# Kernel tuning notes

Measured on AMD Instinct MI355X. Metric: run time of the kernel, lower is better.

## Reference

```python
import jax, jax.numpy as jnp
import numpy as np

B, L, VOCAB = 131072, 256, 40


def setup_inputs() -> dict:
    key = jax.random.key(0)
    x = jax.random.randint(key, (B, L), 0, VOCAB, dtype=jnp.int32)
    return {"x": x}


def reference(x):
    # x: [B, L] int ids, 0 = padding/invalid. Original compacts each row to its
    # nonzero elements (order-preserving) and compares adjacent compacted elems.
    mask = x != 0                                   # [B, L]
    n = mask.sum(axis=-1)                           # [B] valid length per row
    # Stable argsort of the boolean 'is-zero' key moves nonzeros to the front
    # while preserving their relative order == seq[seq != 0] compaction.
    order = jnp.argsort(~mask, axis=-1, stable=True)
    c = jnp.take_along_axis(x, order, axis=-1)      # [B, L] compacted, zeros at tail

    Lm = x.shape[-1]
    pos1 = jnp.arange(Lm - 1)
    pair_valid = pos1[None, :] < (n[:, None] - 1)   # adjacent pairs within valid prefix
    a, b = c[:, :-1], c[:, 1:]
    rep = ((a == b) & pair_valid).sum(axis=-1)
    inc = ((b > a) & pair_valid).sum(axis=-1)
    dec = ((b < a) & pair_valid).sum(axis=-1)
    denom1 = jnp.maximum(n - 1, 1)

    pos2 = jnp.arange(Lm - 2)
    p2_valid = pos2[None, :] < (n[:, None] - 2)     # lag-2 pairs within valid prefix
    per = ((c[:, :-2] == c[:, 2:]) & p2_valid).sum(axis=-1)
    denom2 = jnp.maximum(n - 2, 1)

    repeat_ratio = (rep / denom1).astype(jnp.float32)
    inc_ratio = (inc / denom1).astype(jnp.float32)
    dec_ratio = (dec / denom1).astype(jnp.float32)
    periodicity = jnp.where(n >= 4, (per / denom2).astype(jnp.float32), 0.0)

    feats = jnp.stack([repeat_ratio, inc_ratio, dec_ratio, periodicity], axis=-1)  # [B, 4]
    # Rows with <= 1 valid element produce all-zero features.
    return jnp.where((n > 1)[:, None], feats, 0.0)
```

## Files before the change

kernel.cpp:

```cpp
#include <hip/hip_runtime.h>


constexpr int L_SEQ = 256;
constexpr int WPB   = 4;

__global__ __launch_bounds__(256, 4)
void pattern_kernel(const int* __restrict__ x, float* __restrict__ out, int rows)
{
    __shared__ int c_sh[WPB][L_SEQ];

    const int tid  = threadIdx.x;
    const int wave = tid >> 6;
    const int lane = tid & 63;
    const int row  = blockIdx.x * WPB + wave;
    const bool valid_row = (row < rows);
    const int  rr  = valid_row ? row : 0;

    const int4 v = ((const int4*)(x + (size_t)rr * L_SEQ))[lane];
    int vals[4] = { v.x, v.y, v.z, v.w };

    unsigned long long m0 = __ballot(vals[0] != 0);
    unsigned long long m1 = __ballot(vals[1] != 0);
    unsigned long long m2 = __ballot(vals[2] != 0);
    unsigned long long m3 = __ballot(vals[3] != 0);

    int below = 0;
    below = __builtin_amdgcn_mbcnt_hi((unsigned)(m0 >> 32),
            __builtin_amdgcn_mbcnt_lo((unsigned)m0, below));
    below = __builtin_amdgcn_mbcnt_hi((unsigned)(m1 >> 32),
            __builtin_amdgcn_mbcnt_lo((unsigned)m1, below));
    below = __builtin_amdgcn_mbcnt_hi((unsigned)(m2 >> 32),
            __builtin_amdgcn_mbcnt_lo((unsigned)m2, below));
    below = __builtin_amdgcn_mbcnt_hi((unsigned)(m3 >> 32),
            __builtin_amdgcn_mbcnt_lo((unsigned)m3, below));

    const int n = __popcll(m0) + __popcll(m1) + __popcll(m2) + __popcll(m3);

    int pos = below;
    int* const c = c_sh[wave];
    #pragma unroll
    for (int j = 0; j < 4; ++j) {
        if (vals[j] != 0) c[pos++] = vals[j];
    }

    __asm__ volatile("s_waitcnt lgkmcnt(0)" ::: "memory");

    const int base = lane * 4;
    const int4 q = ((const int4*)c)[lane];
    const int e0 = __shfl_down(q.x, 1, 64);
    const int e1 = __shfl_down(q.y, 1, 64);
    const int a0[6] = { q.x, q.y, q.z, q.w, e0, e1 };

    int packed = 0;
    #pragma unroll
    for (int j = 0; j < 4; ++j) {
        const int i  = base + j;
        const int a  = a0[j];
        const int b  = a0[j + 1];
        const int c2 = a0[j + 2];
        if (i < n - 1) {
            packed += (a == b) ? 1          : 0;
            packed += (b >  a) ? (1 << 8)   : 0;
            packed += (b <  a) ? (1 << 16)  : 0;
            if (i < n - 2) packed += (a == c2) ? (1 << 24) : 0;
        }
    }

    int vsum = packed;
    int t;
    t = __builtin_amdgcn_update_dpp(0, vsum, 0x111, 0xF, 0xF, true); vsum += t;
    t = __builtin_amdgcn_update_dpp(0, vsum, 0x112, 0xF, 0xF, true); vsum += t;
    t = __builtin_amdgcn_update_dpp(0, vsum, 0x114, 0xF, 0xE, true); vsum += t;
    t = __builtin_amdgcn_update_dpp(0, vsum, 0x118, 0xF, 0xC, true); vsum += t;
    t = __builtin_amdgcn_update_dpp(0, vsum, 0x142, 0xA, 0xF, true); vsum += t;
    t = __builtin_amdgcn_update_dpp(0, vsum, 0x143, 0xC, 0xF, true); vsum += t;

    if (lane == 63 && valid_row) {
        const int rep =  vsum        & 0xFF;
        const int inc = (vsum >> 8)  & 0xFF;
        const int dec = (vsum >> 16) & 0xFF;
        const int per = (vsum >> 24) & 0xFF;
        float4 o = make_float4(0.f, 0.f, 0.f, 0.f);
        if (n > 1) {
            const float d1 = (float)(n - 1);
            o.x = (float)rep / d1;
            o.y = (float)inc / d1;
            o.z = (float)dec / d1;
            if (n >= 4) o.w = (float)per / (float)(n - 2);
        }
        ((float4*)out)[row] = o;
    }
}

extern "C" void kernel_launch(void* const* d_in, const int* in_sizes, int n_in,
                              void* d_out, int out_size, void* d_ws, size_t ws_size,
                              hipStream_t stream) {
    const int* x  = (const int*)d_in[0];
    float*    out = (float*)d_out;
    const int rows   = in_sizes[0] / L_SEQ;
    const int blocks = (rows + WPB - 1) / WPB;
    pattern_kernel<<<dim3(blocks), dim3(256), 0, stream>>>(x, out, rows);
}
```

Measured before the change: 182.1 us.

## Process sixteen rows per wave with register prefetch and double-buffered LDS

```diff
diff --git a/kernel.cpp b/kernel.cpp
--- a/kernel.cpp
+++ b/kernel.cpp
@@ -3,92 +3,109 @@
 
 constexpr int L_SEQ = 256;
 constexpr int WPB   = 4;
+constexpr int RPW   = 16;
+constexpr int SLICE = L_SEQ + 64;
 
-__global__ __launch_bounds__(256, 4)
+__global__ __launch_bounds__(256, 8)
 void pattern_kernel(const int* __restrict__ x, float* __restrict__ out, int rows)
 {
-    __shared__ int c_sh[WPB][L_SEQ];
+    __shared__ int c_sh[WPB][2][SLICE];
 
     const int tid  = threadIdx.x;
     const int wave = tid >> 6;
     const int lane = tid & 63;
-    const int row  = blockIdx.x * WPB + wave;
-    const bool valid_row = (row < rows);
-    const int  rr  = valid_row ? row : 0;
+    const long wid = (long)blockIdx.x * WPB + wave;
+    const long row0 = wid * RPW;
+    if (row0 >= rows) return;
 
-    const int4 v = ((const int4*)(x + (size_t)rr * L_SEQ))[lane];
-    int vals[4] = { v.x, v.y, v.z, v.w };
+    const int4* __restrict__ p = (const int4*)x + row0 * (L_SEQ / 4) + lane;
 
-    unsigned long long m0 = __ballot(vals[0] != 0);
-    unsigned long long m1 = __ballot(vals[1] != 0);
-    unsigned long long m2 = __ballot(vals[2] != 0);
-    unsigned long long m3 = __ballot(vals[3] != 0);
+    int4 cur = *p;
 
-    int below = 0;
-    below = __builtin_amdgcn_mbcnt_hi((unsigned)(m0 >> 32),
-            __builtin_amdgcn_mbcnt_lo((unsigned)m0, below));
-    below = __builtin_amdgcn_mbcnt_hi((unsigned)(m1 >> 32),
-            __builtin_amdgcn_mbcnt_lo((unsigned)m1, below));
-    below = __builtin_amdgcn_mbcnt_hi((unsigned)(m2 >> 32),
-            __builtin_amdgcn_mbcnt_lo((unsigned)m2, below));
-    below = __builtin_amdgcn_mbcnt_hi((unsigned)(m3 >> 32),
-            __builtin_amdgcn_mbcnt_lo((unsigned)m3, below));
+    for (int r = 0; r < RPW; ++r) {
+        const long row = row0 + r;
+        if (row >= rows) break;
 
-    const int n = __popcll(m0) + __popcll(m1) + __popcll(m2) + __popcll(m3);
+        int4 nxt = cur;
+        if (r + 1 < RPW && row + 1 < rows) nxt = p[(r + 1) * (L_SEQ / 4)];
 
-    int pos = below;
-    int* const c = c_sh[wave];
-    #pragma unroll
-    for (int j = 0; j < 4; ++j) {
-        if (vals[j] != 0) c[pos++] = vals[j];
-    }
+        const int vals[4] = { cur.x, cur.y, cur.z, cur.w };
 
-    __asm__ volatile("s_waitcnt lgkmcnt(0)" ::: "memory");
+        const unsigned long long m0 = __ballot(vals[0] != 0);
+        const unsigned long long m1 = __ballot(vals[1] != 0);
+        const unsigned long long m2 = __ballot(vals[2] != 0);
+        const unsigned long long m3 = __ballot(vals[3] != 0);
 
-    const int base = lane * 4;
-    const int4 q = ((const int4*)c)[lane];
-    const int e0 = __shfl_down(q.x, 1, 64);
-    const int e1 = __shfl_down(q.y, 1, 64);
-    const int a0[6] = { q.x, q.y, q.z, q.w, e0, e1 };
+        int below = 0;
+        below = __builtin_amdgcn_mbcnt_hi((unsigned)(m0 >> 32),
+                __builtin_amdgcn_mbcnt_lo((unsigned)m0, below));
+        below = __builtin_amdgcn_mbcnt_hi((unsigned)(m1 >> 32),
+                __builtin_amdgcn_mbcnt_lo((unsigned)m1, below));
+        below = __builtin_amdgcn_mbcnt_hi((unsigned)(m2 >> 32),
+                __builtin_amdgcn_mbcnt_lo((unsigned)m2, below));
+        below = __builtin_amdgcn_mbcnt_hi((unsigned)(m3 >> 32),
+                __builtin_amdgcn_mbcnt_lo((unsigned)m3, below));
 
-    int packed = 0;
-    #pragma unroll
-    for (int j = 0; j < 4; ++j) {
-        const int i  = base + j;
-        const int a  = a0[j];
-        const int b  = a0[j + 1];
-        const int c2 = a0[j + 2];
-        if (i < n - 1) {
-            packed += (a == b) ? 1          : 0;
-            packed += (b >  a) ? (1 << 8)   : 0;
-            packed += (b <  a) ? (1 << 16)  : 0;
-            if (i < n - 2) packed += (a == c2) ? (1 << 24) : 0;
+        const int n = __popcll(m0) + __popcll(m1) + __popcll(m2) + __popcll(m3);
+
+        int* const c = c_sh[wave][r & 1];
+        int pos = below;
+        #pragma unroll
+        for (int j = 0; j < 4; ++j) {
+            const bool nz  = (vals[j] != 0);
+            const int addr = nz ? pos : (L_SEQ + lane);
+            c[addr] = vals[j];
+            pos += nz ? 1 : 0;
         }
-    }
+        __asm__ volatile("s_waitcnt lgkmcnt(0)" ::: "memory");
 
-    int vsum = packed;
-    int t;
-    t = __builtin_amdgcn_update_dpp(0, vsum, 0x111, 0xF, 0xF, true); vsum += t;
-    t = __builtin_amdgcn_update_dpp(0, vsum, 0x112, 0xF, 0xF, true); vsum += t;
-    t = __builtin_amdgcn_update_dpp(0, vsum, 0x114, 0xF, 0xE, true); vsum += t;
-    t = __builtin_amdgcn_update_dpp(0, vsum, 0x118, 0xF, 0xC, true); vsum += t;
-    t = __builtin_amdgcn_update_dpp(0, vsum, 0x142, 0xA, 0xF, true); vsum += t;
-    t = __builtin_amdgcn_update_dpp(0, vsum, 0x143, 0xC, 0xF, true); vsum += t;
+        const int base = lane * 4;
+        const int4 q = ((const int4*)c)[lane];
+        const int e0 = __shfl_down(q.x, 1, 64);
+        const int e1 = __shfl_down(q.y, 1, 64);
+        const int a0[6] = { q.x, q.y, q.z, q.w, e0, e1 };
 
-    if (lane == 63 && valid_row) {
-        const int rep =  vsum        & 0xFF;
-        const int inc = (vsum >> 8)  & 0xFF;
-        const int dec = (vsum >> 16) & 0xFF;
-        const int per = (vsum >> 24) & 0xFF;
-        float4 o = make_float4(0.f, 0.f, 0.f, 0.f);
-        if (n > 1) {
-            const float d1 = (float)(n - 1);
-            o.x = (float)rep / d1;
-            o.y = (float)inc / d1;
-            o.z = (float)dec / d1;
-            if (n >= 4) o.w = (float)per / (float)(n - 2);
+        int packed = 0;
+        #pragma unroll
+        for (int j = 0; j < 4; ++j) {
+            const int i  = base + j;
+            const int a  = a0[j];
+            const int b  = a0[j + 1];
+            const int c2 = a0[j + 2];
+            if (i < n - 1) {
+                packed += (a == b) ? 1         : 0;
+                packed += (b >  a) ? (1 << 8)  : 0;
+                packed += (b <  a) ? (1 << 16) : 0;
+                if (i < n - 2) packed += (a == c2) ? (1 << 24) : 0;
+            }
         }
-        ((float4*)out)[row] = o;
+
+        int vsum = packed;
+        int t;
+        t = __builtin_amdgcn_update_dpp(0, vsum, 0x111, 0xF, 0xF, true); vsum += t;
+        t = __builtin_amdgcn_update_dpp(0, vsum, 0x112, 0xF, 0xF, true); vsum += t;
+        t = __builtin_amdgcn_update_dpp(0, vsum, 0x114, 0xF, 0xE, true); vsum += t;
+        t = __builtin_amdgcn_update_dpp(0, vsum, 0x118, 0xF, 0xC, true); vsum += t;
+        t = __builtin_amdgcn_update_dpp(0, vsum, 0x142, 0xA, 0xF, true); vsum += t;
+        t = __builtin_amdgcn_update_dpp(0, vsum, 0x143, 0xC, 0xF, true); vsum += t;
+
+        if (lane == 63) {
+            const int rep =  vsum        & 0xFF;
+            const int inc = (vsum >> 8)  & 0xFF;
+            const int dec = (vsum >> 16) & 0xFF;
+            const int per = (vsum >> 24) & 0xFF;
+            float4 o = make_float4(0.f, 0.f, 0.f, 0.f);
+            if (n > 1) {
+                const float d1 = (float)(n - 1);
+                o.x = (float)rep / d1;
+                o.y = (float)inc / d1;
+                o.z = (float)dec / d1;
+                if (n >= 4) o.w = (float)per / (float)(n - 2);
+            }
+            ((float4*)out)[row] = o;
+        }
+
+        cur = nxt;
     }
 }
 
@@ -97,7 +114,8 @@
                               hipStream_t stream) {
     const int* x  = (const int*)d_in[0];
     float*    out = (float*)d_out;
-    const int rows   = in_sizes[0] / L_SEQ;
-    const int blocks = (rows + WPB - 1) / WPB;
+    const int rows = in_sizes[0] / L_SEQ;
+    const int rows_per_block = WPB * RPW;
+    const int blocks = (rows + rows_per_block - 1) / rows_per_block;
     pattern_kernel<<<dim3(blocks), dim3(256), 0, stream>>>(x, out, rows);
 }
```

New measurement: 189.1 us. 1.04x slower.
